# Performance work log

Measured on AMD Instinct MI355X. Metric: run time of the kernel, lower is better.

The kernel has to match this reference:

```python
import jax, jax.numpy as jnp
import numpy as np

D = 256          # node_embedding_dim (= GRU hidden per direction)
N = 1024         # number of frame nodes
C = 5            # num_classes
COUNTS = [15, 40, 15]   # num_intervals_per_scale
BINS = [80, 60, 80]     # dist_bins_list
MAX_T = 512      # fixed pad length for per-interval sequences (jit-static)


def _quant(w):
    # int8 per-tensor symmetric fake-quant with straight-through estimator
    s = jnp.maximum(jnp.max(jnp.abs(w)) / 127.0, 1e-8)
    q = jnp.clip(jnp.round(w / s), -128, 127) * s
    return w + jax.lax.stop_gradient(q - w)


def _gru_dir(x, eff, wih, whh, bih, bhh):
    # x: [I, T, D] packed-at-front sequences, eff: [I] valid lengths (>=1)
    # masked scan == torch packed GRU final hidden state
    I, T, _ = x.shape
    H = whh.shape[1]
    valid = jnp.arange(T)[None, :] < eff[:, None]   # [I, T]

    def step(h, inp):
        x_t, v = inp                                # [I,D], [I]
        gi = x_t @ wih.T + bih                      # [I, 3H]
        gh = h @ whh.T + bhh
        ir, iz, inn = jnp.split(gi, 3, axis=1)
        hr, hz, hn = jnp.split(gh, 3, axis=1)
        r = jax.nn.sigmoid(ir + hr)
        z = jax.nn.sigmoid(iz + hz)
        n = jnp.tanh(inn + r * hn)
        h = jnp.where(v[:, None], (1.0 - z) * n + z * h, h)
        return h, None

    h0 = jnp.zeros((I, H), x.dtype)
    hF, _ = jax.lax.scan(step, h0, (jnp.swapaxes(x, 0, 1), valid.T))
    return hF


def _forward(node_embeddings, time_positions, node_pred, audio_len, anchor_intervals,
             gru_wih, gru_whh, gru_bih, gru_bhh, w1, w2,
             w3_s0, w3_s1, w3_s2, sw_s0, ew_s0, sw_s1, ew_s1, sw_s2, ew_s2):
    al = audio_len[0]
    tpos = time_positions[:, 0] * al                     # [N]
    abn = jax.nn.softmax(node_pred, axis=-1)[:, 0]       # abnormal scores [N]
    w3s = [w3_s0, w3_s1, w3_s2]
    sws = [sw_s0, sw_s1, sw_s2]
    ews = [ew_s0, ew_s1, ew_s2]
    offs = np.concatenate([[0], np.cumsum(COUNTS)])
    bounds, confs, clss = [], [], []
    for si in range(3):
        I, b = COUNTS[si], BINS[si]
        anc = anchor_intervals[offs[si]:offs[si + 1]]    # [I, 2]
        starts, ends = anc[:, 0], anc[:, 1]
        # interval membership mask [I, N]
        mask = (tpos[None, :] >= starts[:, None]) & (tpos[None, :] <= ends[:, None])
        # compact valid nodes to the front (stable, preserves node order like x[mask])
        order = jnp.argsort(jnp.logical_not(mask), axis=1, stable=True)[:, :MAX_T]
        msort = jnp.take_along_axis(mask, order, axis=1)
        x_loc = node_embeddings[order] * msort[..., None]   # [I, MAX_T, D]; empty -> zeros row
        eff = jnp.clip(mask.sum(axis=1), 1, MAX_T)          # empty interval behaves as one zero step
        hf = _gru_dir(x_loc, eff, gru_wih[si, 0], gru_whh[si, 0], gru_bih[si, 0], gru_bhh[si, 0])
        # backward direction: reverse each valid prefix
        rev_idx = jnp.clip(eff[:, None] - 1 - jnp.arange(MAX_T)[None, :], 0, MAX_T - 1)
        x_rev = jnp.take_along_axis(x_loc, rev_idx[..., None], axis=1)
        hb = _gru_dir(x_rev, eff, gru_wih[si, 1], gru_whh[si, 1], gru_bih[si, 1], gru_bhh[si, 1])
        # shared feature: [2D | abnormal | center | width | 4 zero pads] = 2D+7
        feat = jnp.concatenate([
            hf, hb,
            abn[:I, None],
            ((starts + ends) * 0.5 / al)[:, None],
            ((ends - starts) / al)[:, None],
            jnp.zeros((I, 4), hf.dtype),
        ], axis=1)
        h = jax.nn.relu(feat @ _quant(w1[si]).T)   # dropout = identity (eval)
        h = jax.nn.relu(h @ _quant(w2[si]).T)
        out = h @ _quant(w3s[si]).T                # [I, 2b+1+(C-1)]
        so = jnp.sum(jax.nn.softmax(out[:, :b], axis=1) * sws[si], axis=1)
        eo = jnp.sum(jax.nn.softmax(out[:, b:2 * b], axis=1) * ews[si], axis=1)
        bounds.append(jnp.stack([jnp.clip(starts + so, 0.0, al), jnp.clip(ends + eo, 0.0, al)], axis=1))
        confs.append(out[:, 2 * b])
        clss.append(out[:, 2 * b + 1:])
    return (jnp.concatenate(bounds, axis=0),   # final_bounds [70, 2]
            jnp.concatenate(confs, axis=0),    # interval_conf_logits [70]
            jnp.concatenate(clss, axis=0))     # interval_cls_logits [70, 4]


def setup_inputs() -> dict:
    key = jax.random.key(0)
    ks = jax.random.split(key, 16)
    inp = {}
    inp["node_embeddings"] = jax.random.normal(ks[0], (N, D), jnp.float32)
    inp["time_positions"] = jax.random.uniform(ks[1], (N, 1), dtype=jnp.float32)
    inp["node_pred"] = jax.random.normal(ks[2], (N, C), jnp.float32)
    inp["audio_len"] = jnp.ones((1,), jnp.float32)
    rng = np.random.default_rng(0)
    widths = [0.05, 0.12, 0.30]
    rows = []
    for c, w in zip(COUNTS, widths):
        s = rng.uniform(0.0, 1.0 - w, size=c).astype(np.float32)
        e = s + rng.uniform(0.5 * w, w, size=c).astype(np.float32)
        rows.append(np.stack([s, e], axis=1))
    inp["anchor_intervals"] = jnp.asarray(np.concatenate(rows, axis=0))
    H = D
    def u(k, shape, fan):
        lim = 1.0 / np.sqrt(fan)
        return jax.random.uniform(k, shape, jnp.float32, -lim, lim)
    # GRU params stacked over [scale, direction]
    inp["gru_wih"] = u(ks[3], (3, 2, 3 * H, D), H)
    inp["gru_whh"] = u(ks[4], (3, 2, 3 * H, H), H)
    inp["gru_bih"] = u(ks[5], (3, 2, 3 * H), H)
    inp["gru_bhh"] = u(ks[6], (3, 2, 3 * H), H)
    F_in = 2 * D + 7
    inp["w1"] = u(ks[7], (3, 256, F_in), F_in)
    inp["w2"] = u(ks[8], (3, 256, 256), 256)
    inp["w3_s0"] = u(ks[9], (2 * BINS[0] + 1 + (C - 1), 256), 256)
    inp["w3_s1"] = u(ks[10], (2 * BINS[1] + 1 + (C - 1), 256), 256)
    inp["w3_s2"] = u(ks[11], (2 * BINS[2] + 1 + (C - 1), 256), 256)
    for i, nb in enumerate(BINS):
        inp[f"sw_s{i}"] = jnp.linspace(-20.0, 20.0, nb, dtype=jnp.float32)
        inp[f"ew_s{i}"] = jnp.linspace(-20.0, 20.0, nb, dtype=jnp.float32)
    return inp


def reference(node_embeddings, time_positions, node_pred, audio_len, anchor_intervals,
              gru_wih, gru_whh, gru_bih, gru_bhh, w1, w2,
              w3_s0, w3_s1, w3_s2, sw_s0, ew_s0, sw_s1, ew_s1, sw_s2, ew_s2):
    return _forward(node_embeddings, time_positions, node_pred, audio_len, anchor_intervals,
                    gru_wih, gru_whh, gru_bih, gru_bhh, w1, w2,
                    w3_s0, w3_s1, w3_s2, sw_s0, ew_s0, sw_s1, ew_s1, sw_s2, ew_s2)
```

## Files before the change

### kernel.cpp

```cpp
#include <hip/hip_runtime.h>
#include <math.h>

#define NN 1024
#define NNP 1025
#define DD 256
#define CC 5
#define G3 768
#define MAXT 512
#define NA 70

typedef _Float16 v8h __attribute__((ext_vector_type(8)));
typedef _Float16 v4h __attribute__((ext_vector_type(4)));
typedef float v4f __attribute__((ext_vector_type(4)));
typedef int v4i __attribute__((ext_vector_type(4)));

#define NF1 (3*16*17*64)
#define NF2 (3*16*8*64)
#define NF3 (3*11*8*64)

__device__ __forceinline__ float sigf(float x){ return __fdividef(1.f, 1.f + __expf(-x)); }
__device__ __forceinline__ float tanhf_fast(float x){ return 1.f - __fdividef(2.f, __expf(2.f*x) + 1.f); }

__global__ __launch_bounds__(256) void mega_kernel(
    const float* __restrict__ node_pred, const float* __restrict__ tp_in,
    const float* __restrict__ audio_len, const float* __restrict__ anchors,
    const float* __restrict__ whh, const float* __restrict__ wih,
    const float* __restrict__ emb,
    const float* __restrict__ bih, const float* __restrict__ bhh,
    const float* __restrict__ w1, const float* __restrict__ w2,
    const float* __restrict__ w30, const float* __restrict__ w31, const float* __restrict__ w32,
    float* __restrict__ abn, int* __restrict__ order, int* __restrict__ cnteff,
    float* __restrict__ qs, float* __restrict__ cm,
    uint4* __restrict__ whhB8, _Float16* __restrict__ E){
  __shared__ __align__(16) unsigned char smem[16*264*2];
  int b = blockIdx.x, tid = threadIdx.x;
  if (b < 4){
    int i = b*256 + tid;
    float pv[CC]; float m = -1e30f;
    for (int c=0;c<CC;++c){ pv[c]=node_pred[i*CC+c]; m=fmaxf(m,pv[c]); }
    float s=0.f;
    for (int c=0;c<CC;++c) s += expf(pv[c]-m);
    abn[i] = expf(pv[0]-m)/s;
  } else if (b < 74){
    if (tid >= 64) return;
    int a = b-4; int lane = tid;
    float al = audio_len[0];
    float s = anchors[2*a], e = anchors[2*a+1];
    int* ord = order + a*MAXT;
    int cnt = 0;
    for (int base=0; base<NN; base+=64){
      float tp = tp_in[base+lane]*al;
      bool msk = (tp>=s)&&(tp<=e);
      unsigned long long bal = __ballot(msk);
      int off = (int)__popcll(bal & ((1ull<<lane)-1ull));
      if (msk && (cnt+off)<MAXT) ord[cnt+off] = base+lane;
      cnt += (int)__popcll(bal);
    }
    if (lane==0){ int c = cnt<MAXT?cnt:MAXT; cnteff[2*a]=c; cnteff[2*a+1]=(c>0)?c:1; }
  } else if (b < 83){
    int m = b-74;
    const float* p; int n;
    if (m<3){ p = w1 + (size_t)m*256*519; n = 256*519; }
    else if (m<6){ p = w2 + (size_t)(m-3)*256*256; n = 256*256; }
    else { p = (m==6)?w30:((m==7)?w31:w32); n = ((m==7)?125:165)*256; }
    float mx = 0.f;
    for (int i=tid;i<n;i+=256) mx = fmaxf(mx, fabsf(p[i]));
    float* red = (float*)smem;
    red[tid]=mx; __syncthreads();
    for (int sft=128; sft>0; sft>>=1){ if (tid<sft) red[tid]=fmaxf(red[tid],red[tid+sft]); __syncthreads(); }
    if (tid==0) qs[m] = fmaxf(red[0]/127.f, 1e-8f);
  } else if (b < 101){
    int i = (b-83)*256 + tid;
    if (i >= 4608) return;
    int gt = i % 3; int c = (i/3)&255; int sd = i/768;
    int j = gt*256 + c;
    float v = bih[sd*G3+j] + ((gt<2)? bhh[sd*G3+j] : 0.f);
    E[((size_t)(sd*NNP + NN))*1024 + c*4 + gt] = (_Float16)v;
  } else if (b < 125){
    int bb = b-101;
    int sd = bb>>2, w = bb&3;
    float* cm_lds = (float*)smem;
    int lane = tid & 63, wv = tid >> 6;
    for (int it=0; it<48; ++it){
      int lr = it*4 + wv;
      int gt = lr>>6, cc = lr&63;
      int j = gt*256 + w*64 + cc;
      float4 v = reinterpret_cast<const float4*>(whh + ((size_t)sd*G3 + j)*DD)[lane];
      float mx = fmaxf(fmaxf(fabsf(v.x),fabsf(v.y)), fmaxf(fabsf(v.z),fabsf(v.w)));
      #pragma unroll
      for (int sh=1; sh<64; sh<<=1) mx = fmaxf(mx, __shfl_xor(mx, sh));
      if (lane==0){
        float cmax = fmaxf(mx, 1e-12f);
        cm_lds[lr] = cmax;
        cm[sd*G3 + j] = cmax;
      }
    }
    __syncthreads();
    #pragma unroll
    for (int ee=0; ee<12; ++ee){
      int il = tid*12 + ee;
      int lane2 = il/48; int rr = il - lane2*48;
      int nt = rr>>2; int q = rr&3;
      int gt = nt>>2, s = nt&3;
      int j  = gt*256 + w*64 + s*16 + (lane2&15);
      int lr = gt*64  + s*16 + (lane2&15);
      int kbase = 64*q + 16*(lane2>>4);
      float inv = 127.f/cm_lds[lr];
      const float* src = whh + ((size_t)sd*G3 + j)*DD + kbase;
      unsigned int dw[4];
      #pragma unroll
      for (int d2=0; d2<4; ++d2){
        unsigned int acc = 0;
        #pragma unroll
        for (int e2=0; e2<4; ++e2){
          float qv = rintf(src[4*d2+e2]*inv);
          qv = fminf(fmaxf(qv,-127.f),127.f);
          int iq = (int)qv;
          acc |= ((unsigned int)(iq & 255)) << (8*e2);
        }
        dw[d2] = acc;
      }
      uint4 v; v.x=dw[0]; v.y=dw[1]; v.z=dw[2]; v.w=dw[3];
      whhB8[(size_t)(sd*4 + w)*3072 + il] = v;
    }
  } else {
    typedef _Float16 AsT[264];
    AsT* As = (AsT*)smem;
    int b2 = b - 125;
    int sd = b2 / 768;
    int rem = b2 - sd*768;
    int r_t = rem & 63, cg = rem >> 6;
    int row0 = r_t*16;
    int lane = tid & 63, wv = tid >> 6;
    int l15 = lane & 15, g16 = lane >> 4;
    {
      int rr = tid>>4, k0 = (tid&15)*16;
      const float4* ep = reinterpret_cast<const float4*>(emb + (size_t)(row0+rr)*DD + k0);
      #pragma unroll
      for (int f=0; f<4; ++f){
        float4 v = ep[f];
        v4h o; o[0]=(_Float16)v.x; o[1]=(_Float16)v.y; o[2]=(_Float16)v.z; o[3]=(_Float16)v.w;
        *reinterpret_cast<v4h*>(&As[rr][k0 + f*4]) = o;
      }
    }
    __syncthreads();
    int c_t = cg*4 + wv;
    int j = c_t*16 + l15;
    const float* Bp = wih + ((size_t)sd*G3 + j)*DD + 8*g16;
    float bsum = bih[sd*G3 + j] + (((j>>8) < 2) ? bhh[sd*G3 + j] : 0.f);
    v4f acc = {0.f,0.f,0.f,0.f};
    #pragma unroll
    for (int q=0;q<8;++q){
      v8h af = *reinterpret_cast<const v8h*>(&As[l15][32*q + 8*g16]);
      float4 b0 = *reinterpret_cast<const float4*>(Bp + 32*q);
      float4 b1 = *reinterpret_cast<const float4*>(Bp + 32*q + 4);
      v8h bf;
      bf[0]=(_Float16)b0.x; bf[1]=(_Float16)b0.y; bf[2]=(_Float16)b0.z; bf[3]=(_Float16)b0.w;
      bf[4]=(_Float16)b1.x; bf[5]=(_Float16)b1.y; bf[6]=(_Float16)b1.z; bf[7]=(_Float16)b1.w;
      acc = __builtin_amdgcn_mfma_f32_16x16x32_f16(af, bf, acc, 0,0,0);
    }
    int gt = j>>8, c = j&255;
    #pragma unroll
    for (int r=0;r<4;++r){
      int row = row0 + g16*4 + r;
      E[((size_t)(sd*NNP + row))*1024 + c*4 + gt] = (_Float16)(acc[r] + bsum);
    }
  }
}

__global__ __launch_bounds__(256, 1) void gru_kernel(
    const _Float16* __restrict__ E, const v4i* __restrict__ whhB8,
    const float* __restrict__ bhh, const float* __restrict__ cm,
    const int* __restrict__ order, const int* __restrict__ cnteff,
    float* __restrict__ hout,
    const float* __restrict__ w1, const float* __restrict__ w2,
    const float* __restrict__ w30, const float* __restrict__ w31, const float* __restrict__ w32,
    const float* __restrict__ qs,
    v8h* __restrict__ w1F, v8h* __restrict__ w2F, v8h* __restrict__ w3F){
  int blk = blockIdx.x;
  int tid = threadIdx.x;
  if (blk >= NA*2){
    int i = (blk - NA*2)*256 + tid;
    if (i < NF1){
      int lane = i & 63; int rest = i >> 6;
      int q = rest % 17; int rc = rest / 17;
      int ct = rc & 15; int si = rc >> 4;
      int j = ct*16 + (lane&15);
      int k0 = q*32 + 8*(lane>>4);
      float inv = 1.f/qs[si];
      const float* src = w1 + ((size_t)(si*256 + j))*519;
      v8h o;
      #pragma unroll
      for (int e=0;e<8;++e){
        int k = k0+e;
        float wv = (k<519)? src[k] : 0.f;
        float qv = rintf(wv*inv);
        qv = fminf(fmaxf(qv,-128.f),127.f);
        o[e] = (_Float16)qv;
      }
      w1F[i] = o;
    } else if (i < NF1+NF2){
      int r = i - NF1;
      int lane = r & 63; int rest = r >> 6;
      int q = rest & 7; int rc = rest >> 3;
      int ct = rc & 15; int si = rc >> 4;
      int j = ct*16 + (lane&15);
      int k0 = q*32 + 8*(lane>>4);
      float inv = 1.f/qs[3+si];
      const float* src = w2 + ((size_t)(si*256 + j))*256 + k0;
      v8h o;
      #pragma unroll
      for (int e=0;e<8;++e){
        float qv = rintf(src[e]*inv);
        qv = fminf(fmaxf(qv,-128.f),127.f);
        o[e] = (_Float16)qv;
      }
      w2F[r] = o;
    } else if (i < NF1+NF2+NF3){
      int r = i - NF1 - NF2;
      int lane = r & 63; int rest = r >> 6;
      int q = rest & 7; int rc = rest >> 3;
      int ct = rc % 11; int si = rc / 11;
      int j = ct*16 + (lane&15);
      int nout = (si==1)?125:165;
      const float* w3 = (si==0)?w30:((si==1)?w31:w32);
      int k0 = q*32 + 8*(lane>>4);
      float inv = 1.f/qs[6+si];
      v8h o;
      #pragma unroll
      for (int e=0;e<8;++e){
        float wv = (j<nout)? w3[(size_t)j*256 + k0+e] : 0.f;
        float qv = rintf(wv*inv);
        qv = fminf(fmaxf(qv,-128.f),127.f);
        o[e] = (_Float16)qv;
      }
      w3F[r] = o;
    }
    return;
  }
  int a = blk>>1, d = blk&1;
  int si = (a<15)?0:((a<55)?1:2);
  int sd = si*2+d;
  int w = tid>>6, lane = tid&63;
  int g16 = lane>>4, l15 = lane&15;

  __shared__ int ord_s[MAXT];
  __shared__ alignas(16) signed char h8[2][DD];

  ord_s[tid]     = order[a*MAXT + tid];
  ord_s[tid+256] = order[a*MAXT + tid + 256];
  h8[0][tid] = 0;

  int cnt = cnteff[2*a], eff = cnteff[2*a+1];

  int c = w*64 + g16*16 + l15;
  float bn = bhh[sd*G3 + 2*DD + c];
  const float ISQ = 1.f/(127.f*127.f);
  float sr = cm[sd*G3 +       c]*ISQ;
  float sz = cm[sd*G3 + 256 + c]*ISQ;
  float sn = cm[sd*G3 + 512 + c]*ISQ;

  v4i bf[12][4];
  {
    const v4i* wp = whhB8 + (((size_t)sd*4 + w)*64 + lane)*48;
    #pragma unroll
    for (int nt=0;nt<12;++nt)
      #pragma unroll
      for (int q=0;q<4;++q)
        bf[nt][q] = wp[nt*4+q];
  }

  const uint2* Eb = reinterpret_cast<const uint2*>(E) + (size_t)sd*NNP*256;

  __syncthreads();

  float h = 0.f;
  uint2 gEven, gOdd;
  {
    int idx0 = d ? (eff-1) : 0;
    int n0 = (idx0 < cnt) ? ord_s[idx0] : NN;
    gEven = Eb[(size_t)n0*256 + c];
  }

  for (int t=0;t<eff;++t){
    int p = t & 1;
    if (t+1 < eff){
      int idx1 = d ? (eff-2-t) : (t+1);
      int n1 = (idx1 < cnt) ? ord_s[idx1] : NN;
      if (p==0) gOdd  = Eb[(size_t)n1*256 + c];
      else      gEven = Eb[(size_t)n1*256 + c];
    }
    v4i a0={0,0,0,0}, a1={0,0,0,0}, a2={0,0,0,0}, a3={0,0,0,0};
    v4i a4={0,0,0,0}, a5={0,0,0,0}, a6={0,0,0,0}, a7={0,0,0,0};
    v4i a8={0,0,0,0}, a9={0,0,0,0}, a10={0,0,0,0}, a11={0,0,0,0};
    #pragma unroll
    for (int q=0;q<4;++q){
      v4i af = *reinterpret_cast<const v4i*>(&h8[p][64*q + 16*g16]);
      a0  = __builtin_amdgcn_mfma_i32_16x16x64_i8(af, bf[0][q],  a0,  0,0,0);
      a1  = __builtin_amdgcn_mfma_i32_16x16x64_i8(af, bf[1][q],  a1,  0,0,0);
      a2  = __builtin_amdgcn_mfma_i32_16x16x64_i8(af, bf[2][q],  a2,  0,0,0);
      a3  = __builtin_amdgcn_mfma_i32_16x16x64_i8(af, bf[3][q],  a3,  0,0,0);
      a4  = __builtin_amdgcn_mfma_i32_16x16x64_i8(af, bf[4][q],  a4,  0,0,0);
      a5  = __builtin_amdgcn_mfma_i32_16x16x64_i8(af, bf[5][q],  a5,  0,0,0);
      a6  = __builtin_amdgcn_mfma_i32_16x16x64_i8(af, bf[6][q],  a6,  0,0,0);
      a7  = __builtin_amdgcn_mfma_i32_16x16x64_i8(af, bf[7][q],  a7,  0,0,0);
      a8  = __builtin_amdgcn_mfma_i32_16x16x64_i8(af, bf[8][q],  a8,  0,0,0);
      a9  = __builtin_amdgcn_mfma_i32_16x16x64_i8(af, bf[9][q],  a9,  0,0,0);
      a10 = __builtin_amdgcn_mfma_i32_16x16x64_i8(af, bf[10][q], a10, 0,0,0);
      a11 = __builtin_amdgcn_mfma_i32_16x16x64_i8(af, bf[11][q], a11, 0,0,0);
    }
    v4h ev = __builtin_bit_cast(v4h, (p==0) ? gEven : gOdd);
    int ir  = (g16==0)?a0[0]:((g16==1)?a1[0]:((g16==2)?a2[0]:a3[0]));
    int iz  = (g16==0)?a4[0]:((g16==1)?a5[0]:((g16==2)?a6[0]:a7[0]));
    int inn = (g16==0)?a8[0]:((g16==1)?a9[0]:((g16==2)?a10[0]:a11[0]));
    float r  = sigf((float)ev[0] + (float)ir*sr);
    float z  = sigf((float)ev[1] + (float)iz*sz);
    float nv = tanhf_fast((float)ev[2] + r*((float)inn*sn + bn));
    h = z*(h - nv) + nv;
    h8[p^1][c] = (signed char)(int)rintf(h*127.f);
    __syncthreads();
  }
  hout[(size_t)(2*a+d)*DD + c] = h;
}

__global__ __launch_bounds__(512) void mlp_kernel(
    const float* __restrict__ hout, const float* __restrict__ abn,
    const float* __restrict__ anchors, const float* __restrict__ audio_len,
    const v8h* __restrict__ w1F, const v8h* __restrict__ w2F, const v8h* __restrict__ w3F,
    const float* __restrict__ qs,
    const float* __restrict__ sw0, const float* __restrict__ ew0,
    const float* __restrict__ sw1, const float* __restrict__ ew1,
    const float* __restrict__ sw2, const float* __restrict__ ew2,
    float* __restrict__ out){
  int bm = blockIdx.x;
  int si = (bm==0)?0:((bm<4)?1:2);
  int mt = (bm==0)?0:((bm<4)?(bm-1):0);
  int cntA = (si==1)?40:15;
  int offA = (si==0)?0:((si==1)?15:55);
  int bb   = (si==1)?60:80;
  int m0 = mt*16;
  const float* sw = (si==0)?sw0:((si==1)?sw1:sw2);
  const float* ew = (si==0)?ew0:((si==1)?ew1:ew2);
  float al = audio_len[0];

  __shared__ _Float16 feat[16][552];
  __shared__ _Float16 h1s[16][264];
  __shared__ float    os[16][184];

  int tid = threadIdx.x;
  int lane = tid & 63, wv = tid >> 6;
  int l15 = lane & 15, g16 = lane >> 4;

  for (int idx = tid; idx < 16*552; idx += 512){
    int r = idx / 552, c2 = idx - r*552;
    float v = 0.f;
    int m = m0 + r;
    if (m < cntA){
      int a = offA + m;
      if (c2 < 256)       v = hout[(size_t)(2*a)*DD + c2];
      else if (c2 < 512)  v = hout[(size_t)(2*a+1)*DD + (c2-256)];
      else if (c2 == 512) v = abn[m];
      else if (c2 == 513){ float s=anchors[2*a], e=anchors[2*a+1]; v = (s+e)*0.5f/al; }
      else if (c2 == 514){ float s=anchors[2*a], e=anchors[2*a+1]; v = (e-s)/al; }
    }
    feat[r][c2] = (_Float16)v;
  }
  __syncthreads();
  float sc1 = qs[si], sc2 = qs[3+si], sc3 = qs[6+si];

  for (int nt = wv; nt < 16; nt += 8){
    int j = nt*16 + l15;
    const v8h* bp = w1F + (size_t)(si*16 + nt)*17*64 + lane;
    v4f acc = {0.f,0.f,0.f,0.f};
    for (int kq = 0; kq < 17; ++kq){
      v8h af = *reinterpret_cast<const v8h*>(&feat[l15][kq*32 + 8*g16]);
      acc = __builtin_amdgcn_mfma_f32_16x16x32_f16(af, bp[kq*64], acc, 0,0,0);
    }
    #pragma unroll
    for (int r=0;r<4;++r) h1s[g16*4+r][j] = (_Float16)fmaxf(acc[r]*sc1, 0.f);
  }
  __syncthreads();
  for (int nt = wv; nt < 16; nt += 8){
    int j = nt*16 + l15;
    const v8h* bp = w2F + (size_t)(si*16 + nt)*8*64 + lane;
    v4f acc = {0.f,0.f,0.f,0.f};
    for (int kq = 0; kq < 8; ++kq){
      v8h af = *reinterpret_cast<const v8h*>(&h1s[l15][kq*32 + 8*g16]);
      acc = __builtin_amdgcn_mfma_f32_16x16x32_f16(af, bp[kq*64], acc, 0,0,0);
    }
    #pragma unroll
    for (int r=0;r<4;++r) feat[g16*4+r][j] = (_Float16)fmaxf(acc[r]*sc2, 0.f);
  }
  __syncthreads();
  for (int nt = wv; nt < 11; nt += 8){
    int j = nt*16 + l15;
    const v8h* bp = w3F + (size_t)(si*11 + nt)*8*64 + lane;
    v4f acc = {0.f,0.f,0.f,0.f};
    for (int kq = 0; kq < 8; ++kq){
      v8h af = *reinterpret_cast<const v8h*>(&feat[l15][kq*32 + 8*g16]);
      acc = __builtin_amdgcn_mfma_f32_16x16x32_f16(af, bp[kq*64], acc, 0,0,0);
    }
    #pragma unroll
    for (int r=0;r<4;++r) os[g16*4+r][j] = acc[r]*sc3;
  }
  __syncthreads();
  for (int lm = wv; lm < 16; lm += 8){
    int m = m0 + lm;
    if (m >= cntA) continue;
    int a = offA + m;
    float s = anchors[2*a], e = anchors[2*a+1];
    float x0 = (lane < bb) ? os[lm][lane] : -1e30f;
    float x1 = (lane+64 < bb) ? os[lm][lane+64] : -1e30f;
    float mx = fmaxf(x0, x1);
    #pragma unroll
    for (int sh=1; sh<64; sh<<=1) mx = fmaxf(mx, __shfl_xor(mx, sh));
    float e0 = (lane < bb) ? expf(x0-mx) : 0.f;
    float e1 = (lane+64 < bb) ? expf(x1-mx) : 0.f;
    float se = e0 + e1;
    float ws2 = e0*((lane<bb)?sw[lane]:0.f) + e1*((lane+64<bb)?sw[lane+64]:0.f);
    #pragma unroll
    for (int sh=1; sh<64; sh<<=1){ se += __shfl_xor(se, sh); ws2 += __shfl_xor(ws2, sh); }
    float so = ws2/se;
    float y0 = (lane < bb) ? os[lm][bb+lane] : -1e30f;
    float y1 = (lane+64 < bb) ? os[lm][bb+lane+64] : -1e30f;
    float my = fmaxf(y0, y1);
    #pragma unroll
    for (int sh=1; sh<64; sh<<=1) my = fmaxf(my, __shfl_xor(my, sh));
    float f0 = (lane < bb) ? expf(y0-my) : 0.f;
    float f1 = (lane+64 < bb) ? expf(y1-my) : 0.f;
    float sf = f0 + f1;
    float wf = f0*((lane<bb)?ew[lane]:0.f) + f1*((lane+64<bb)?ew[lane+64]:0.f);
    #pragma unroll
    for (int sh=1; sh<64; sh<<=1){ sf += __shfl_xor(sf, sh); wf += __shfl_xor(wf, sh); }
    float eo = wf/sf;
    if (lane == 0){
      out[2*a]   = fminf(fmaxf(s+so, 0.f), al);
      out[2*a+1] = fminf(fmaxf(e+eo, 0.f), al);
      out[140+a] = os[lm][2*bb];
    }
    if (lane < 4) out[210+4*a+lane] = os[lm][2*bb+1+lane];
  }
}

extern "C" void kernel_launch(void* const* d_in, const int* in_sizes, int n_in,
                              void* d_out, int out_size, void* d_ws, size_t ws_size,
                              hipStream_t stream){
  const float* emb   = (const float*)d_in[0];
  const float* tpin  = (const float*)d_in[1];
  const float* npred = (const float*)d_in[2];
  const float* alen  = (const float*)d_in[3];
  const float* anch  = (const float*)d_in[4];
  const float* wih   = (const float*)d_in[5];
  const float* whh   = (const float*)d_in[6];
  const float* bih   = (const float*)d_in[7];
  const float* bhh   = (const float*)d_in[8];
  const float* w1    = (const float*)d_in[9];
  const float* w2    = (const float*)d_in[10];
  const float* w30   = (const float*)d_in[11];
  const float* w31   = (const float*)d_in[12];
  const float* w32   = (const float*)d_in[13];
  const float* sw0   = (const float*)d_in[14];
  const float* ew0   = (const float*)d_in[15];
  const float* sw1   = (const float*)d_in[16];
  const float* ew1   = (const float*)d_in[17];
  const float* sw2   = (const float*)d_in[18];
  const float* ew2   = (const float*)d_in[19];

  char* ws = (char*)d_ws;
  size_t off = 0;
  auto take = [&](size_t bytes)->char*{
    char* p = ws + off;
    off = (off + bytes + 255) & ~(size_t)255;
    return p;
  };
  float* abn    = (float*)take((size_t)NN*4);
  int*   order_ = (int*)  take((size_t)NA*MAXT*4);
  int*   cnteff = (int*)  take((size_t)NA*2*4);
  float* qs     = (float*)take(16*4);
  float* cm     = (float*)take((size_t)6*G3*4);
  uint4* whhB8  = (uint4*)take((size_t)6*4*3072*16);
  _Float16* E   = (_Float16*)take((size_t)6*NNP*1024*2);
  float* hout   = (float*)take((size_t)NA*2*DD*4);
  v8h* w1F      = (v8h*)take((size_t)NF1*16);
  v8h* w2F      = (v8h*)take((size_t)NF2*16);
  v8h* w3F      = (v8h*)take((size_t)NF3*16);
  (void)ws_size; (void)in_sizes; (void)n_in; (void)out_size;

  mega_kernel<<<dim3(4733), dim3(256), 0, stream>>>(npred, tpin, alen, anch, whh, wih, emb,
                                                    bih, bhh, w1, w2, w30, w31, w32,
                                                    abn, order_, cnteff, qs, cm, whhB8, E);
  {
    const int packBlocks = (NF1+NF2+NF3+255)/256;
    gru_kernel<<<dim3(NA*2 + packBlocks), dim3(256), 0, stream>>>(
        E, (const v4i*)whhB8, bhh, cm, order_, cnteff, hout,
        w1, w2, w30, w31, w32, qs, w1F, w2F, w3F);
  }
  mlp_kernel<<<dim3(5), dim3(512), 0, stream>>>(hout, abn, anch, alen, w1F, w2F, w3F, qs,
                                                sw0, ew0, sw1, ew1, sw2, ew2, (float*)d_out);
}
```

Baseline: 410.1 us.

## Split GRU recurrence across 8 waves with 32 hidden columns each

Each GRU sequence block now uses 512 threads in 8 wavefronts, and each wave owns 32 hidden columns instead of 64. The int8 recurrent-weight packing is relaid out to match, so each wave issues 6 MFMA tiles per k-chunk instead of 12. This halves the serial per-step MFMA chain and the register-held weights per wave, aiming to shorten the latency-bound recurrent loop. In exchange, half of the lanes in each wave compute duplicate results, and the per-step block barrier now synchronises twice as many waves.

```diff
diff --git a/kernel.cpp b/kernel.cpp
--- a/kernel.cpp
+++ b/kernel.cpp
@@ -17,6 +17,7 @@
 #define NF1 (3*16*17*64)
 #define NF2 (3*16*8*64)
 #define NF3 (3*11*8*64)
+#define NFT (NF1+NF2+NF3)
 
 __device__ __forceinline__ float sigf(float x){ return __fdividef(1.f, 1.f + __expf(-x)); }
 __device__ __forceinline__ float tanhf_fast(float x){ return 1.f - __fdividef(2.f, __expf(2.f*x) + 1.f); }
@@ -76,15 +77,15 @@
     int j = gt*256 + c;
     float v = bih[sd*G3+j] + ((gt<2)? bhh[sd*G3+j] : 0.f);
     E[((size_t)(sd*NNP + NN))*1024 + c*4 + gt] = (_Float16)v;
-  } else if (b < 125){
+  } else if (b < 149){
     int bb = b-101;
-    int sd = bb>>2, w = bb&3;
+    int sd = bb>>3, w = bb&7;
     float* cm_lds = (float*)smem;
     int lane = tid & 63, wv = tid >> 6;
-    for (int it=0; it<48; ++it){
+    for (int it=0; it<24; ++it){
       int lr = it*4 + wv;
-      int gt = lr>>6, cc = lr&63;
-      int j = gt*256 + w*64 + cc;
+      int gt = lr>>5, c = lr&31;
+      int j = gt*256 + w*32 + c;
       float4 v = reinterpret_cast<const float4*>(whh + ((size_t)sd*G3 + j)*DD)[lane];
       float mx = fmaxf(fmaxf(fabsf(v.x),fabsf(v.y)), fmaxf(fabsf(v.z),fabsf(v.w)));
       #pragma unroll
@@ -97,13 +98,14 @@
     }
     __syncthreads();
     #pragma unroll
-    for (int ee=0; ee<12; ++ee){
-      int il = tid*12 + ee;
-      int lane2 = il/48; int rr = il - lane2*48;
-      int nt = rr>>2; int q = rr&3;
-      int gt = nt>>2, s = nt&3;
-      int j  = gt*256 + w*64 + s*16 + (lane2&15);
-      int lr = gt*64  + s*16 + (lane2&15);
+    for (int ee=0; ee<6; ++ee){
+      int il = tid*6 + ee;
+      int q    = il & 3;
+      int nt   = (il>>2) % 6;
+      int lane2= il / 24;
+      int gt = nt>>1, half = nt&1;
+      int j  = gt*256 + w*32 + half*16 + (lane2&15);
+      int lr = gt*32  + half*16 + (lane2&15);
       int kbase = 64*q + 16*(lane2>>4);
       float inv = 127.f/cm_lds[lr];
       const float* src = whh + ((size_t)sd*G3 + j)*DD + kbase;
@@ -121,12 +123,12 @@
         dw[d2] = acc;
       }
       uint4 v; v.x=dw[0]; v.y=dw[1]; v.z=dw[2]; v.w=dw[3];
-      whhB8[(size_t)(sd*4 + w)*3072 + il] = v;
+      whhB8[(size_t)(sd*8 + w)*1536 + il] = v;
     }
   } else {
     typedef _Float16 AsT[264];
     AsT* As = (AsT*)smem;
-    int b2 = b - 125;
+    int b2 = b - 149;
     int sd = b2 / 768;
     int rem = b2 - sd*768;
     int r_t = rem & 63, cg = rem >> 6;
@@ -168,7 +170,7 @@
   }
 }
 
-__global__ __launch_bounds__(256, 1) void gru_kernel(
+__global__ __launch_bounds__(512, 2) void gru_kernel(
     const _Float16* __restrict__ E, const v4i* __restrict__ whhB8,
     const float* __restrict__ bhh, const float* __restrict__ cm,
     const int* __restrict__ order, const int* __restrict__ cnteff,
@@ -180,7 +182,7 @@
   int blk = blockIdx.x;
   int tid = threadIdx.x;
   if (blk >= NA*2){
-    int i = (blk - NA*2)*256 + tid;
+    int i = (blk - NA*2)*512 + tid;
     if (i < NF1){
       int lane = i & 63; int rest = i >> 6;
       int q = rest % 17; int rc = rest / 17;
@@ -216,7 +218,7 @@
         o[e] = (_Float16)qv;
       }
       w2F[r] = o;
-    } else if (i < NF1+NF2+NF3){
+    } else if (i < NFT){
       int r = i - NF1 - NF2;
       int lane = r & 63; int rest = r >> 6;
       int q = rest & 7; int rc = rest >> 3;
@@ -242,29 +244,29 @@
   int si = (a<15)?0:((a<55)?1:2);
   int sd = si*2+d;
   int w = tid>>6, lane = tid&63;
-  int g16 = lane>>4, l15 = lane&15;
+  int g16 = lane>>4;
+  int ct = g16 & 1;
 
   __shared__ int ord_s[MAXT];
   __shared__ alignas(16) signed char h8[2][DD];
 
-  ord_s[tid]     = order[a*MAXT + tid];
-  ord_s[tid+256] = order[a*MAXT + tid + 256];
-  h8[0][tid] = 0;
+  ord_s[tid] = order[a*MAXT + tid];
+  if (tid < DD) h8[0][tid] = 0;
 
   int cnt = cnteff[2*a], eff = cnteff[2*a+1];
 
-  int c = w*64 + g16*16 + l15;
+  int c = w*32 + (lane&31);
   float bn = bhh[sd*G3 + 2*DD + c];
   const float ISQ = 1.f/(127.f*127.f);
-  float sr = cm[sd*G3 +       c]*ISQ;
-  float sz = cm[sd*G3 + 256 + c]*ISQ;
-  float sn = cm[sd*G3 + 512 + c]*ISQ;
-
-  v4i bf[12][4];
+  float sr = cm[sd*G3 +        c]*ISQ;
+  float sz = cm[sd*G3 + 256 +  c]*ISQ;
+  float sn = cm[sd*G3 + 512 +  c]*ISQ;
+
+  v4i bf[6][4];
   {
-    const v4i* wp = whhB8 + (((size_t)sd*4 + w)*64 + lane)*48;
-    #pragma unroll
-    for (int nt=0;nt<12;++nt)
+    const v4i* wp = whhB8 + (((size_t)sd*8 + w)*64 + lane)*24;
+    #pragma unroll
+    for (int nt=0;nt<6;++nt)
       #pragma unroll
       for (int q=0;q<4;++q)
         bf[nt][q] = wp[nt*4+q];
@@ -290,37 +292,30 @@
       if (p==0) gOdd  = Eb[(size_t)n1*256 + c];
       else      gEven = Eb[(size_t)n1*256 + c];
     }
-    v4i a0={0,0,0,0}, a1={0,0,0,0}, a2={0,0,0,0}, a3={0,0,0,0};
-    v4i a4={0,0,0,0}, a5={0,0,0,0}, a6={0,0,0,0}, a7={0,0,0,0};
-    v4i a8={0,0,0,0}, a9={0,0,0,0}, a10={0,0,0,0}, a11={0,0,0,0};
+    v4i acc0={0,0,0,0}, acc1={0,0,0,0}, acc2={0,0,0,0};
+    v4i acc3={0,0,0,0}, acc4={0,0,0,0}, acc5={0,0,0,0};
     #pragma unroll
     for (int q=0;q<4;++q){
       v4i af = *reinterpret_cast<const v4i*>(&h8[p][64*q + 16*g16]);
-      a0  = __builtin_amdgcn_mfma_i32_16x16x64_i8(af, bf[0][q],  a0,  0,0,0);
-      a1  = __builtin_amdgcn_mfma_i32_16x16x64_i8(af, bf[1][q],  a1,  0,0,0);
-      a2  = __builtin_amdgcn_mfma_i32_16x16x64_i8(af, bf[2][q],  a2,  0,0,0);
-      a3  = __builtin_amdgcn_mfma_i32_16x16x64_i8(af, bf[3][q],  a3,  0,0,0);
-      a4  = __builtin_amdgcn_mfma_i32_16x16x64_i8(af, bf[4][q],  a4,  0,0,0);
-      a5  = __builtin_amdgcn_mfma_i32_16x16x64_i8(af, bf[5][q],  a5,  0,0,0);
-      a6  = __builtin_amdgcn_mfma_i32_16x16x64_i8(af, bf[6][q],  a6,  0,0,0);
-      a7  = __builtin_amdgcn_mfma_i32_16x16x64_i8(af, bf[7][q],  a7,  0,0,0);
-      a8  = __builtin_amdgcn_mfma_i32_16x16x64_i8(af, bf[8][q],  a8,  0,0,0);
-      a9  = __builtin_amdgcn_mfma_i32_16x16x64_i8(af, bf[9][q],  a9,  0,0,0);
-      a10 = __builtin_amdgcn_mfma_i32_16x16x64_i8(af, bf[10][q], a10, 0,0,0);
-      a11 = __builtin_amdgcn_mfma_i32_16x16x64_i8(af, bf[11][q], a11, 0,0,0);
+      acc0 = __builtin_amdgcn_mfma_i32_16x16x64_i8(af, bf[0][q], acc0, 0,0,0);
+      acc1 = __builtin_amdgcn_mfma_i32_16x16x64_i8(af, bf[1][q], acc1, 0,0,0);
+      acc2 = __builtin_amdgcn_mfma_i32_16x16x64_i8(af, bf[2][q], acc2, 0,0,0);
+      acc3 = __builtin_amdgcn_mfma_i32_16x16x64_i8(af, bf[3][q], acc3, 0,0,0);
+      acc4 = __builtin_amdgcn_mfma_i32_16x16x64_i8(af, bf[4][q], acc4, 0,0,0);
+      acc5 = __builtin_amdgcn_mfma_i32_16x16x64_i8(af, bf[5][q], acc5, 0,0,0);
     }
     v4h ev = __builtin_bit_cast(v4h, (p==0) ? gEven : gOdd);
-    int ir  = (g16==0)?a0[0]:((g16==1)?a1[0]:((g16==2)?a2[0]:a3[0]));
-    int iz  = (g16==0)?a4[0]:((g16==1)?a5[0]:((g16==2)?a6[0]:a7[0]));
-    int inn = (g16==0)?a8[0]:((g16==1)?a9[0]:((g16==2)?a10[0]:a11[0]));
+    int ir  = (ct==0) ? acc0[0] : acc1[0];
+    int iz  = (ct==0) ? acc2[0] : acc3[0];
+    int inn = (ct==0) ? acc4[0] : acc5[0];
     float r  = sigf((float)ev[0] + (float)ir*sr);
     float z  = sigf((float)ev[1] + (float)iz*sz);
     float nv = tanhf_fast((float)ev[2] + r*((float)inn*sn + bn));
     h = z*(h - nv) + nv;
-    h8[p^1][c] = (signed char)(int)rintf(h*127.f);
+    if (lane < 32) h8[p^1][c] = (signed char)(int)rintf(h*127.f);
     __syncthreads();
   }
-  hout[(size_t)(2*a+d)*DD + c] = h;
+  if (lane < 32) hout[(size_t)(2*a+d)*DD + c] = h;
 }
 
 __global__ __launch_bounds__(512) void mlp_kernel(
@@ -478,7 +473,7 @@
   int*   cnteff = (int*)  take((size_t)NA*2*4);
   float* qs     = (float*)take(16*4);
   float* cm     = (float*)take((size_t)6*G3*4);
-  uint4* whhB8  = (uint4*)take((size_t)6*4*3072*16);
+  uint4* whhB8  = (uint4*)take((size_t)6*8*1536*16);
   _Float16* E   = (_Float16*)take((size_t)6*NNP*1024*2);
   float* hout   = (float*)take((size_t)NA*2*DD*4);
   v8h* w1F      = (v8h*)take((size_t)NF1*16);
@@ -486,12 +481,12 @@
   v8h* w3F      = (v8h*)take((size_t)NF3*16);
   (void)ws_size; (void)in_sizes; (void)n_in; (void)out_size;
 
-  mega_kernel<<<dim3(4733), dim3(256), 0, stream>>>(npred, tpin, alen, anch, whh, wih, emb,
+  mega_kernel<<<dim3(4757), dim3(256), 0, stream>>>(npred, tpin, alen, anch, whh, wih, emb,
                                                     bih, bhh, w1, w2, w30, w31, w32,
                                                     abn, order_, cnteff, qs, cm, whhB8, E);
   {
-    const int packBlocks = (NF1+NF2+NF3+255)/256;
-    gru_kernel<<<dim3(NA*2 + packBlocks), dim3(256), 0, stream>>>(
+    const int packBlocks = (NFT + 511)/512;
+    gru_kernel<<<dim3(NA*2 + packBlocks), dim3(512), 0, stream>>>(
         E, (const v4i*)whhB8, bhh, cm, order_, cnteff, hout,
         w1, w2, w30, w31, w32, qs, w1F, w2F, w3F);
   }
```

Result: faster. 389.0 us (-5.2%).
